# Performance work log

Hardware: AMD Instinct MI355X
Metric: run time of the kernel (lower is better)

Reference implementation:

```python
import jax, jax.numpy as jnp
import numpy as np

N = 20000      # nodes
E = 640000     # edges (avg degree 32)
F = 6          # feature_dim
D = 128        # weight_dim
L = 3          # lstm num_layers
DEPTH = 10     # extra iterations after initial call


def setup_inputs() -> dict:
    key = jax.random.key(0)
    ks = jax.random.split(key, 10)
    s = 0.05
    return {
        "features": jax.random.normal(ks[0], (N, F), jnp.float32),
        "src": jax.random.randint(ks[1], (E,), 0, N),
        "dst": jax.random.randint(ks[2], (E,), 0, N),
        "W_in": jax.random.normal(ks[3], (F, D), jnp.float32) * s,
        "b_in": jnp.zeros((D,), jnp.float32),
        "Wih0": jax.random.normal(ks[4], (4 * D, 2 * D), jnp.float32) * s,   # layer 0: input = concat(h_in, feat)
        "Wih_rest": jax.random.normal(ks[5], (2, 4 * D, D), jnp.float32) * s,  # layers 1,2
        "Whh": jax.random.normal(ks[6], (L, 4 * D, D), jnp.float32) * s,
        "bih": jnp.zeros((L, 4 * D), jnp.float32),
        "bhh": jnp.zeros((L, 4 * D), jnp.float32),
        "W_out": jax.random.normal(ks[7], (D, 1), jnp.float32) * s,
        "b_out": jnp.zeros((1,), jnp.float32),
    }


def _lstm_cell(x, h, c, Wih, Whh, b):
    # PyTorch gate order: i, f, g, o
    gates = x @ Wih.T + h @ Whh.T + b              # [N, 4D]
    i, f, g, o = jnp.split(gates, 4, axis=-1)
    i = jax.nn.sigmoid(i)
    f = jax.nn.sigmoid(f)
    o = jax.nn.sigmoid(o)
    g = jnp.tanh(g)
    c_new = f * c + i * g
    h_new = o * jnp.tanh(c_new)
    return h_new, c_new


def reference(features, src, dst, W_in, b_in, Wih0, Wih_rest, Whh, bih, bhh, W_out, b_out):
    n = features.shape[0]
    b = bih + bhh                                   # [L, 4D]

    def agg(x):
        # DGL update_all(copy_src, mean): mean over incoming edges (src -> dst)
        s = jax.ops.segment_sum(x[src], dst, num_segments=n)
        deg = jax.ops.segment_sum(jnp.ones((src.shape[0],), x.dtype), dst, num_segments=n)
        return jnp.where(deg[:, None] > 0, s / jnp.maximum(deg, 1.0)[:, None], 0.0)

    feat = jax.nn.relu(features @ W_in + b_in)      # [N, D]
    h = jnp.zeros((L, n, D), features.dtype)
    c = jnp.zeros((L, n, D), features.dtype)

    def step(carry, _):
        feat, h, c = carry
        x0 = jnp.concatenate([agg(feat), feat], axis=-1)   # [N, 2D]
        h0, c0 = _lstm_cell(x0, h[0], c[0], Wih0, Whh[0], b[0])
        h1, c1 = _lstm_cell(h0, h[1], c[1], Wih_rest[0], Whh[1], b[1])
        h2, c2 = _lstm_cell(h1, h[2], c[2], Wih_rest[1], Whh[2], b[2])
        return (h2, jnp.stack([h0, h1, h2]), jnp.stack([c0, c1, c2])), None

    # initial call + depth extra iterations, all structurally identical
    (feat, h, c), _ = jax.lax.scan(step, (feat, h, c), None, length=1 + DEPTH)
    return h[-1] @ W_out + b_out                    # [N, 1]
```

## Files before the change

### kernel.cpp

```cpp
#include <hip/hip_runtime.h>
#include <math.h>

typedef _Float16 f16;
typedef __attribute__((ext_vector_type(8))) _Float16 half8;
typedef __attribute__((ext_vector_type(4))) float float4v;

__device__ __forceinline__ float fast_sigmoid(float x) { return 1.0f / (1.0f + __expf(-x)); }
__device__ __forceinline__ float fast_tanh(float x) {
    float a = fabsf(x);
    float e = __expf(-2.0f * a);
    float t = (1.0f - e) / (1.0f + e);
    return copysignf(t, x);
}

__device__ __forceinline__ void async_copy16(const void* gsrc, void* ldst) {
    __builtin_amdgcn_global_load_lds(
        (const __attribute__((address_space(1))) void*)gsrc,
        (__attribute__((address_space(3))) void*)ldst,
        16, 0, 0);
}

__global__ void packb_kernel(const float* __restrict__ Wih, int Kih,
                             const float* __restrict__ Whh, int K,
                             const float* __restrict__ bih, const float* __restrict__ bhh,
                             f16* __restrict__ Bp, float* __restrict__ bp) {
    int t = blockIdx.x * blockDim.x + threadIdx.x;
    if (t >= (K << 9)) return;
    int colp = t / K;
    int k = t - colp * K;
    int dg = colp >> 6, q = (colp >> 4) & 3, dl = colp & 15;
    int j = q * 128 + dg * 16 + dl;
    float v = (k < Kih) ? Wih[j * Kih + k] : Whh[j * (K - Kih) + (k - Kih)];
    Bp[t] = (f16)v;
    if (k == 0) bp[colp] = bih[j] + bhh[j];
}

__global__ void feat0_kernel(const float* __restrict__ features, const float* __restrict__ W_in,
                             const float* __restrict__ b_in, f16* __restrict__ feat, int n) {
    int t = blockIdx.x * blockDim.x + threadIdx.x;
    if (t >= n * 128) return;
    int node = t >> 7;
    int d = t & 127;
    float s = b_in[d];
#pragma unroll
    for (int k = 0; k < 6; ++k) s += features[node * 6 + k] * W_in[k * 128 + d];
    feat[t] = (f16)fmaxf(s, 0.0f);
}

__global__ void hist_kernel(const int* __restrict__ dst, int* __restrict__ cnt, int e) {
    int t = blockIdx.x * blockDim.x + threadIdx.x;
    if (t < e) atomicAdd(&cnt[dst[t]], 1);
}

__global__ void scan_kernel(const int* __restrict__ cnt, int* __restrict__ off,
                            int* __restrict__ cur, float* __restrict__ recip, int n) {
    __shared__ int wsum[16];
    __shared__ int stot;
    int t = threadIdx.x;
    int lane = t & 63, wv = t >> 6;
    int R = 0;
    int rounds = (n + 1023) >> 10;
    for (int i = 0; i < rounds; ++i) {
        int idx = (i << 10) + t;
        int v = (idx < n) ? cnt[idx] : 0;
        int s = v;
#pragma unroll
        for (int o = 1; o < 64; o <<= 1) {
            int u = __shfl_up(s, o, 64);
            if (lane >= o) s += u;
        }
        if (lane == 63) wsum[wv] = s;
        __syncthreads();
        if (t == 0) {
            int a = 0;
#pragma unroll
            for (int j = 0; j < 16; ++j) { int x = wsum[j]; wsum[j] = a; a += x; }
            stot = a;
        }
        __syncthreads();
        int excl = R + wsum[wv] + s - v;
        if (idx < n) {
            off[idx] = excl; cur[idx] = excl;
            recip[idx] = (v > 0) ? 1.0f / (float)v : 0.0f;
        }
        R += stot;
        __syncthreads();
    }
    if (t == 0) off[n] = R;
}

__global__ void scatter_kernel(const int* __restrict__ src, const int* __restrict__ dst,
                               int* __restrict__ cur, int* __restrict__ esrc, int e) {
    int t = blockIdx.x * blockDim.x + threadIdx.x;
    if (t >= e) return;
    int d = dst[t];
    int p = atomicAdd(&cur[d], 1);
    esrc[p] = src[t];
}

__global__ __launch_bounds__(256, 6) void agg_kernel(
    const f16* __restrict__ feat, const int* __restrict__ off,
    const int* __restrict__ esrc, const float* __restrict__ recip,
    f16* __restrict__ agg, int n) {
    int slot = threadIdx.x >> 4;
    int lane = threadIdx.x & 15;
    int v = blockIdx.x * 16 + slot;
    if (v >= n) return;
    int e0 = off[v], e1 = off[v + 1];
    float a[8];
#pragma unroll
    for (int j = 0; j < 8; ++j) a[j] = 0.0f;
    int e = e0;
    for (; e + 8 <= e1; e += 8) {
        int ss[8];
#pragma unroll
        for (int u = 0; u < 8; ++u) ss[u] = esrc[e + u];
        half8 vv[8];
#pragma unroll
        for (int u = 0; u < 8; ++u)
            vv[u] = *(const half8*)&feat[(size_t)ss[u] * 128 + lane * 8];
#pragma unroll
        for (int u = 0; u < 8; ++u)
#pragma unroll
            for (int j = 0; j < 8; ++j) a[j] += (float)vv[u][j];
    }
    for (; e < e1; ++e) {
        int s = esrc[e];
        half8 v0 = *(const half8*)&feat[(size_t)s * 128 + lane * 8];
#pragma unroll
        for (int j = 0; j < 8; ++j) a[j] += (float)v0[j];
    }
    float r = recip[v];
    half8 o;
#pragma unroll
    for (int j = 0; j < 8; ++j) o[j] = (f16)(a[j] * r);
    *(half8*)&agg[(size_t)v * 128 + lane * 8] = o;
}

#define BM 64

template <int PARTS>
__global__ __launch_bounds__(256, 3) void gemm_lstm(
    const f16* __restrict__ A0, const f16* __restrict__ A1, const f16* __restrict__ A2,
    const f16* __restrict__ Bp, const float* __restrict__ bp,
    float* __restrict__ c, f16* __restrict__ h_out, int nrows) {
    constexpr int K = PARTS * 128;
    constexpr int NT = PARTS * 4;
    __shared__ f16 As[2][64 * 32];
    __shared__ f16 Bs[2][256 * 32];

    const int tid = threadIdx.x;
    const int w = tid >> 6;
    const int lane = tid & 63;
    const int dl = lane & 15;
    const int quad = lane >> 4;
    const int row0 = blockIdx.x * BM;
    const int cb = blockIdx.y;

    float4v acc[4][4];
#pragma unroll
    for (int q = 0; q < 4; ++q) {
        float b = bp[cb * 256 + w * 64 + q * 16 + dl];
#pragma unroll
        for (int rt = 0; rt < 4; ++rt) {
            acc[rt][q][0] = b; acc[rt][q][1] = b; acc[rt][q][2] = b; acc[rt][q][3] = b;
        }
    }

    const int srow = lane >> 2;
    const int sj = lane & 3;
    const int sg = sj ^ ((srow >> 1) & 3);
    const int rslot = (quad ^ ((dl >> 1) & 3)) << 3;

    auto stage = [&](int kt, int bsel) {
        const f16* Ap = A0;
        const int pi = kt >> 2;
        if (PARTS >= 2 && pi == 1) Ap = A1;
        if (PARTS >= 3 && pi == 2) Ap = A2;
        const int kk = (kt & 3) * 32;
        async_copy16(&Ap[(size_t)(row0 + w * 16 + srow) * 128 + kk + (sg << 3)],
                     (f16*)As[bsel] + w * 512);
        const f16* Bbase = Bp + (size_t)(cb * 256) * K + kt * 32;
#pragma unroll
        for (int i = 0; i < 4; ++i) {
            int m = i * 4 + w;
            async_copy16(&Bbase[(size_t)(m * 16 + srow) * K + (sg << 3)],
                         (f16*)Bs[bsel] + m * 512);
        }
    };

    stage(0, 0);
    __syncthreads();

    for (int kt = 0; kt < NT; ++kt) {
        const int cur = kt & 1;
        if (kt + 1 < NT) stage(kt + 1, cur ^ 1);

        half8 a[4], b[4];
#pragma unroll
        for (int rt = 0; rt < 4; ++rt)
            a[rt] = *(const half8*)&As[cur][(rt * 16 + dl) * 32 + rslot];
#pragma unroll
        for (int q = 0; q < 4; ++q)
            b[q] = *(const half8*)&Bs[cur][((w * 4 + q) * 16 + dl) * 32 + rslot];
#pragma unroll
        for (int rt = 0; rt < 4; ++rt)
#pragma unroll
            for (int q = 0; q < 4; ++q)
                acc[rt][q] = __builtin_amdgcn_mfma_f32_16x16x32_f16(a[rt], b[q], acc[rt][q], 0, 0, 0);

        __syncthreads();
    }

    float* cpriv = c + ((size_t)(blockIdx.x * 2 + cb)) * 4096;
    const int d = cb * 64 + w * 16 + dl;
#pragma unroll
    for (int rt = 0; rt < 4; ++rt) {
        float4v ig = acc[rt][0], fg = acc[rt][1], gg = acc[rt][2], og = acc[rt][3];
        float* cp = cpriv + rt * 1024 + tid * 4;
        float4v cold = *(const float4v*)cp;
        float4v cn;
        float hn[4];
#pragma unroll
        for (int r = 0; r < 4; ++r) {
            float i_ = fast_sigmoid(ig[r]);
            float f_ = fast_sigmoid(fg[r]);
            float g_ = fast_tanh(gg[r]);
            float o_ = fast_sigmoid(og[r]);
            float cv = f_ * cold[r] + i_ * g_;
            cn[r] = cv;
            hn[r] = o_ * fast_tanh(cv);
        }
        *(float4v*)cp = cn;
#pragma unroll
        for (int r = 0; r < 4; ++r) {
            int nr = row0 + rt * 16 + (quad << 2) + r;
            if (nr < nrows) h_out[(size_t)nr * 128 + d] = (f16)hn[r];
        }
    }
}

__global__ void out_kernel(const f16* __restrict__ h2, const float* __restrict__ Wout,
                           const float* __restrict__ bout, float* __restrict__ out) {
    int n = blockIdx.x;
    int l = threadIdx.x;
    float v = (float)h2[(size_t)n * 128 + l] * Wout[l] +
              (float)h2[(size_t)n * 128 + 64 + l] * Wout[64 + l];
#pragma unroll
    for (int o = 32; o > 0; o >>= 1) v += __shfl_down(v, o, 64);
    if (l == 0) out[n] = v + bout[0];
}

extern "C" void kernel_launch(void* const* d_in, const int* in_sizes, int n_in,
                              void* d_out, int out_size, void* d_ws, size_t ws_size,
                              hipStream_t stream) {
    const float* features = (const float*)d_in[0];
    const int*   src      = (const int*)d_in[1];
    const int*   dst      = (const int*)d_in[2];
    const float* W_in     = (const float*)d_in[3];
    const float* b_in     = (const float*)d_in[4];
    const float* Wih0     = (const float*)d_in[5];
    const float* Wih_rest = (const float*)d_in[6];
    const float* Whh      = (const float*)d_in[7];
    const float* bih      = (const float*)d_in[8];
    const float* bhh      = (const float*)d_in[9];
    const float* W_out    = (const float*)d_in[10];
    const float* b_out    = (const float*)d_in[11];
    float* out = (float*)d_out;

    const int N = in_sizes[0] / 6;
    const int E = in_sizes[1];
    const int NP = N + BM;

    char* ws = (char*)d_ws;
    size_t pos = 0;
    auto alloc = [&](size_t bytes) -> void* {
        void* p = ws + pos;
        pos = (pos + bytes + 255) & ~(size_t)255;
        return p;
    };
    const size_t hrow = 128;
    const size_t hbytes = (size_t)NP * hrow * sizeof(f16);
    const size_t cbytes = (size_t)NP * hrow * sizeof(float);
    f16* feath = (f16*)alloc(hbytes);
    f16* aggh  = (f16*)alloc(hbytes);
    f16* hblk  = (f16*)alloc(6 * hbytes);
    f16* hA[3], * hB[3];
    for (int l = 0; l < 3; ++l) {
        hA[l] = hblk + (size_t)l * NP * hrow;
        hB[l] = hblk + (size_t)(l + 3) * NP * hrow;
    }
    float* cblk = (float*)alloc(3 * cbytes);
    float* c0 = cblk + 0 * (size_t)NP * hrow;
    float* c1 = cblk + 1 * (size_t)NP * hrow;
    float* c2 = cblk + 2 * (size_t)NP * hrow;
    f16* Bp0 = (f16*)alloc((size_t)512 * 384 * sizeof(f16));
    f16* Bp1 = (f16*)alloc((size_t)512 * 256 * sizeof(f16));
    f16* Bp2 = (f16*)alloc((size_t)512 * 256 * sizeof(f16));
    float* bp0 = (float*)alloc(512 * sizeof(float));
    float* bp1 = (float*)alloc(512 * sizeof(float));
    float* bp2 = (float*)alloc(512 * sizeof(float));
    int*   cnt   = (int*)alloc((size_t)N * 4);
    int*   offs  = (int*)alloc((size_t)(N + 1) * 4);
    int*   cur   = (int*)alloc((size_t)N * 4);
    int*   esrc  = (int*)alloc((size_t)E * 4);
    float* recip = (float*)alloc((size_t)N * 4);

    hipMemsetAsync(hblk, 0, 6 * hbytes, stream);
    hipMemsetAsync(cblk, 0, 3 * cbytes, stream);
    hipMemsetAsync(cnt, 0, (size_t)N * 4, stream);

    packb_kernel<<<(512 * 384 + 255) / 256, 256, 0, stream>>>(
        Wih0, 256, Whh, 384, bih, bhh, Bp0, bp0);
    packb_kernel<<<(512 * 256 + 255) / 256, 256, 0, stream>>>(
        Wih_rest, 128, Whh + 512 * 128, 256, bih + 512, bhh + 512, Bp1, bp1);
    packb_kernel<<<(512 * 256 + 255) / 256, 256, 0, stream>>>(
        Wih_rest + 512 * 128, 128, Whh + 2 * 512 * 128, 256, bih + 1024, bhh + 1024, Bp2, bp2);

    feat0_kernel<<<(N * 128 + 255) / 256, 256, 0, stream>>>(features, W_in, b_in, feath, N);
    hist_kernel<<<(E + 255) / 256, 256, 0, stream>>>(dst, cnt, E);
    scan_kernel<<<1, 1024, 0, stream>>>(cnt, offs, cur, recip, N);
    scatter_kernel<<<(E + 255) / 256, 256, 0, stream>>>(src, dst, cur, esrc, E);

    const dim3 ggrid((N + BM - 1) / BM, 2, 1);
    const int gagg = (N + 15) / 16;
    const f16* featcur = feath;
    f16 *r0 = hA[0], *r1 = hA[1], *r2 = hA[2];
    f16 *w0 = hB[0], *w1 = hB[1], *w2 = hB[2];
    for (int step = 0; step < 11; ++step) {
        agg_kernel<<<gagg, 256, 0, stream>>>(featcur, offs, esrc, recip, aggh, N);
        gemm_lstm<3><<<ggrid, 256, 0, stream>>>(aggh, featcur, r0, Bp0, bp0, c0, w0, N);
        gemm_lstm<2><<<ggrid, 256, 0, stream>>>(w0, r1, nullptr, Bp1, bp1, c1, w1, N);
        gemm_lstm<2><<<ggrid, 256, 0, stream>>>(w1, r2, nullptr, Bp2, bp2, c2, w2, N);
        featcur = w2;
        f16* t;
        t = r0; r0 = w0; w0 = t;
        t = r1; r1 = w1; w1 = t;
        t = r2; r2 = w2; w2 = t;
    }
    out_kernel<<<N, 64, 0, stream>>>((const f16*)featcur, W_out, b_out, out);
}
```

Before: 1.080 ms.

## Pre-swizzle LSTM weights, skip zero-state work on first step, rework output kernel

The weight-packing kernel now stores B tiles in the exact swizzled LDS order, so each GEMM stage reads weights with contiguous 16-byte copies instead of strided rows. On the first step a FIRST template variant skips the recurrent K-tiles and the cell-state load, since h and c are zero. The large h/c memsets are replaced by small memsets of the padding rows, and launch bounds rise to 4 blocks per CU. The output projection now processes 16 nodes per block with vector loads. The risk is correctness of the new packed layout and of padding rows that are no longer cleared.

```diff
diff --git a/kernel.cpp b/kernel.cpp
--- a/kernel.cpp
+++ b/kernel.cpp
@@ -21,18 +21,25 @@
 }
 
 __global__ void packb_kernel(const float* __restrict__ Wih, int Kih,
-                             const float* __restrict__ Whh, int K,
+                             const float* __restrict__ Whh, int K, int NKT,
                              const float* __restrict__ bih, const float* __restrict__ bhh,
-                             f16* __restrict__ Bp, float* __restrict__ bp) {
+                             f16* __restrict__ Bpk, float* __restrict__ bp) {
     int t = blockIdx.x * blockDim.x + threadIdx.x;
     if (t >= (K << 9)) return;
-    int colp = t / K;
-    int k = t - colp * K;
-    int dg = colp >> 6, q = (colp >> 4) & 3, dl = colp & 15;
+    int e = t & 7;
+    int sj = (t >> 3) & 3;
+    int colp = (t >> 5) & 255;
+    int rest = t >> 13;
+    int kt = rest % NKT;
+    int cb = rest / NKT;
+    int swz = (colp >> 1) & 3;
+    int k = kt * 32 + ((sj ^ swz) << 3) + e;
+    int colq = cb * 256 + colp;
+    int dg = colq >> 6, q = (colq >> 4) & 3, dl = colq & 15;
     int j = q * 128 + dg * 16 + dl;
     float v = (k < Kih) ? Wih[j * Kih + k] : Whh[j * (K - Kih) + (k - Kih)];
-    Bp[t] = (f16)v;
-    if (k == 0) bp[colp] = bih[j] + bhh[j];
+    Bpk[t] = (f16)v;
+    if (kt == 0 && e == 0 && sj == swz) bp[colq] = bih[j] + bhh[j];
 }
 
 __global__ void feat0_kernel(const float* __restrict__ features, const float* __restrict__ W_in,
@@ -139,13 +146,13 @@
 
 #define BM 64
 
-template <int PARTS>
-__global__ __launch_bounds__(256, 3) void gemm_lstm(
+template <int PARTS, bool FIRST>
+__global__ __launch_bounds__(256, 4) void gemm_lstm(
     const f16* __restrict__ A0, const f16* __restrict__ A1, const f16* __restrict__ A2,
-    const f16* __restrict__ Bp, const float* __restrict__ bp,
+    const f16* __restrict__ Bpk, const float* __restrict__ bp,
     float* __restrict__ c, f16* __restrict__ h_out, int nrows) {
-    constexpr int K = PARTS * 128;
-    constexpr int NT = PARTS * 4;
+    constexpr int NKT = PARTS * 4;
+    constexpr int NT = FIRST ? (PARTS - 1) * 4 : PARTS * 4;
     __shared__ f16 As[2][64 * 32];
     __shared__ f16 Bs[2][256 * 32];
 
@@ -171,6 +178,8 @@
     const int sj = lane & 3;
     const int sg = sj ^ ((srow >> 1) & 3);
     const int rslot = (quad ^ ((dl >> 1) & 3)) << 3;
+
+    const f16* Bk0 = Bpk + (size_t)cb * NKT * 8192 + w * 2048 + lane * 8;
 
     auto stage = [&](int kt, int bsel) {
         const f16* Ap = A0;
@@ -180,13 +189,10 @@
         const int kk = (kt & 3) * 32;
         async_copy16(&Ap[(size_t)(row0 + w * 16 + srow) * 128 + kk + (sg << 3)],
                      (f16*)As[bsel] + w * 512);
-        const f16* Bbase = Bp + (size_t)(cb * 256) * K + kt * 32;
-#pragma unroll
-        for (int i = 0; i < 4; ++i) {
-            int m = i * 4 + w;
-            async_copy16(&Bbase[(size_t)(m * 16 + srow) * K + (sg << 3)],
-                         (f16*)Bs[bsel] + m * 512);
-        }
+        const f16* Bsrc = Bk0 + (size_t)kt * 8192;
+#pragma unroll
+        for (int i = 0; i < 4; ++i)
+            async_copy16(Bsrc + i * 512, (f16*)Bs[bsel] + w * 2048 + i * 512);
     };
 
     stage(0, 0);
@@ -218,7 +224,12 @@
     for (int rt = 0; rt < 4; ++rt) {
         float4v ig = acc[rt][0], fg = acc[rt][1], gg = acc[rt][2], og = acc[rt][3];
         float* cp = cpriv + rt * 1024 + tid * 4;
-        float4v cold = *(const float4v*)cp;
+        float4v cold;
+        if (FIRST) {
+            cold[0] = 0.0f; cold[1] = 0.0f; cold[2] = 0.0f; cold[3] = 0.0f;
+        } else {
+            cold = *(const float4v*)cp;
+        }
         float4v cn;
         float hn[4];
 #pragma unroll
@@ -240,15 +251,20 @@
     }
 }
 
-__global__ void out_kernel(const f16* __restrict__ h2, const float* __restrict__ Wout,
-                           const float* __restrict__ bout, float* __restrict__ out) {
-    int n = blockIdx.x;
-    int l = threadIdx.x;
-    float v = (float)h2[(size_t)n * 128 + l] * Wout[l] +
-              (float)h2[(size_t)n * 128 + 64 + l] * Wout[64 + l];
-#pragma unroll
-    for (int o = 32; o > 0; o >>= 1) v += __shfl_down(v, o, 64);
-    if (l == 0) out[n] = v + bout[0];
+__global__ __launch_bounds__(256, 8) void out_kernel(
+    const f16* __restrict__ h2, const float* __restrict__ Wout,
+    const float* __restrict__ bout, float* __restrict__ out, int n) {
+    int grp = threadIdx.x >> 4;
+    int l = threadIdx.x & 15;
+    int node = blockIdx.x * 16 + grp;
+    if (node >= n) return;
+    half8 h = *(const half8*)&h2[(size_t)node * 128 + l * 8];
+    float s = 0.0f;
+#pragma unroll
+    for (int j = 0; j < 8; ++j) s += (float)h[j] * Wout[l * 8 + j];
+#pragma unroll
+    for (int o = 8; o > 0; o >>= 1) s += __shfl_down(s, o, 16);
+    if (l == 0) out[node] = s + bout[0];
 }
 
 extern "C" void kernel_launch(void* const* d_in, const int* in_sizes, int n_in,
@@ -306,16 +322,16 @@
     int*   esrc  = (int*)alloc((size_t)E * 4);
     float* recip = (float*)alloc((size_t)N * 4);
 
-    hipMemsetAsync(hblk, 0, 6 * hbytes, stream);
-    hipMemsetAsync(cblk, 0, 3 * cbytes, stream);
     hipMemsetAsync(cnt, 0, (size_t)N * 4, stream);
+    hipMemsetAsync(feath + (size_t)N * hrow, 0, (size_t)(NP - N) * hrow * sizeof(f16), stream);
+    hipMemsetAsync(aggh + (size_t)N * hrow, 0, (size_t)(NP - N) * hrow * sizeof(f16), stream);
 
     packb_kernel<<<(512 * 384 + 255) / 256, 256, 0, stream>>>(
-        Wih0, 256, Whh, 384, bih, bhh, Bp0, bp0);
+        Wih0, 256, Whh, 384, 12, bih, bhh, Bp0, bp0);
     packb_kernel<<<(512 * 256 + 255) / 256, 256, 0, stream>>>(
-        Wih_rest, 128, Whh + 512 * 128, 256, bih + 512, bhh + 512, Bp1, bp1);
+        Wih_rest, 128, Whh + 512 * 128, 256, 8, bih + 512, bhh + 512, Bp1, bp1);
     packb_kernel<<<(512 * 256 + 255) / 256, 256, 0, stream>>>(
-        Wih_rest + 512 * 128, 128, Whh + 2 * 512 * 128, 256, bih + 1024, bhh + 1024, Bp2, bp2);
+        Wih_rest + 512 * 128, 128, Whh + 2 * 512 * 128, 256, 8, bih + 1024, bhh + 1024, Bp2, bp2);
 
     feat0_kernel<<<(N * 128 + 255) / 256, 256, 0, stream>>>(features, W_in, b_in, feath, N);
     hist_kernel<<<(E + 255) / 256, 256, 0, stream>>>(dst, cnt, E);
@@ -329,14 +345,20 @@
     f16 *w0 = hB[0], *w1 = hB[1], *w2 = hB[2];
     for (int step = 0; step < 11; ++step) {
         agg_kernel<<<gagg, 256, 0, stream>>>(featcur, offs, esrc, recip, aggh, N);
-        gemm_lstm<3><<<ggrid, 256, 0, stream>>>(aggh, featcur, r0, Bp0, bp0, c0, w0, N);
-        gemm_lstm<2><<<ggrid, 256, 0, stream>>>(w0, r1, nullptr, Bp1, bp1, c1, w1, N);
-        gemm_lstm<2><<<ggrid, 256, 0, stream>>>(w1, r2, nullptr, Bp2, bp2, c2, w2, N);
+        if (step == 0) {
+            gemm_lstm<3, true ><<<ggrid, 256, 0, stream>>>(aggh, featcur, r0, Bp0, bp0, c0, w0, N);
+            gemm_lstm<2, true ><<<ggrid, 256, 0, stream>>>(w0, r1, nullptr, Bp1, bp1, c1, w1, N);
+            gemm_lstm<2, true ><<<ggrid, 256, 0, stream>>>(w1, r2, nullptr, Bp2, bp2, c2, w2, N);
+        } else {
+            gemm_lstm<3, false><<<ggrid, 256, 0, stream>>>(aggh, featcur, r0, Bp0, bp0, c0, w0, N);
+            gemm_lstm<2, false><<<ggrid, 256, 0, stream>>>(w0, r1, nullptr, Bp1, bp1, c1, w1, N);
+            gemm_lstm<2, false><<<ggrid, 256, 0, stream>>>(w1, r2, nullptr, Bp2, bp2, c2, w2, N);
+        }
         featcur = w2;
         f16* t;
         t = r0; r0 = w0; w0 = t;
         t = r1; r1 = w1; w1 = t;
         t = r2; r2 = w2; w2 = t;
     }
-    out_kernel<<<N, 64, 0, stream>>>((const f16*)featcur, W_out, b_out, out);
-}
+    out_kernel<<<(N + 15) / 16, 256, 0, stream>>>((const f16*)featcur, W_out, b_out, out, N);
+}
```

After: 1.015 ms, median of 2. -6.1%, faster.
